# Kernel optimization log

Hardware: AMD Instinct MI355X
Metric: run time of the kernel (lower is better)

## Reference

```python
import jax, jax.numpy as jnp
import numpy as np

VOCAB, EMBED, HIDDEN, NCLS = 32000, 512, 1024, 1000
BATCH, SEQ = 128, 512


def setup_inputs() -> dict:
    key = jax.random.key(0)
    ks = jax.random.split(key, 8)
    s_in = 1.0 / np.sqrt(EMBED + HIDDEN)
    s_h = 1.0 / np.sqrt(HIDDEN)
    return {
        "x": jax.random.randint(ks[0], (BATCH, SEQ), 0, VOCAB, dtype=jnp.int32),
        "emb": jax.random.normal(ks[1], (VOCAB, EMBED), dtype=jnp.float32),
        "Wz": jax.random.uniform(ks[2], (EMBED + HIDDEN, HIDDEN), jnp.float32, -s_in, s_in),
        "bz": jax.random.uniform(ks[3], (HIDDEN,), jnp.float32, -s_in, s_in),
        "Wh": jax.random.uniform(ks[4], (EMBED + HIDDEN, HIDDEN), jnp.float32, -s_in, s_in),
        "bh": jax.random.uniform(ks[5], (HIDDEN,), jnp.float32, -s_in, s_in),
        "Wfc": jax.random.uniform(ks[6], (HIDDEN, NCLS), jnp.float32, -s_h, s_h),
        "bfc": jax.random.uniform(ks[7], (NCLS,), jnp.float32, -s_h, s_h),
    }


def reference(x, emb, Wz, bz, Wh, bh, Wfc, bfc):
    # embedding lookup: [B, S, E]
    e = emb[x]
    B = x.shape[0]
    h0 = jnp.zeros((B, Wz.shape[1]), dtype=emb.dtype)

    def step(h, x_t):
        c = jnp.concatenate([x_t, h], axis=1)          # [B, E+H]
        z = jax.nn.sigmoid(c @ Wz + bz)                # forget/update gate
        h_tilde = jnp.tanh(c @ Wh + bh)                # candidate state
        h_new = (1.0 - z) * h + z * h_tilde
        return h_new, None

    h_final, _ = jax.lax.scan(step, h0, jnp.swapaxes(e, 0, 1))  # scan over S
    return h_final @ Wfc + bfc                          # logits [B, NCLS]
```

## Files before the change

kernel.cpp:

```cpp
#include <hip/hip_runtime.h>

#define BATCH 128
#define SEQ   512
#define EMB   512
#define HID   1024
#define NCLS  1000
#define NBLK  128
#define TPB   512

using short8 = __attribute__((ext_vector_type(8))) short;
using f32x4  = __attribute__((ext_vector_type(4))) float;
typedef unsigned long long u64;

__device__ __forceinline__ short f2bf(float f) {
    unsigned u = __float_as_uint(f);
    unsigned r = (u + 0x7fffu + ((u >> 16) & 1u)) >> 16;
    return (short)r;
}
__device__ __forceinline__ float bf2f(short s) {
    unsigned u = ((unsigned)(unsigned short)s) << 16;
    return __uint_as_float(u);
}
__device__ __forceinline__ short8 pack8(float4 a, float4 b) {
    short8 s;
    s[0] = f2bf(a.x); s[1] = f2bf(a.y); s[2] = f2bf(a.z); s[3] = f2bf(a.w);
    s[4] = f2bf(b.x); s[5] = f2bf(b.y); s[6] = f2bf(b.z); s[7] = f2bf(b.w);
    return s;
}
__device__ __forceinline__ short8 mk8(u64 lo, u64 hi) {
    union { u64 d[2]; short8 s; } u;
    u.d[0] = lo; u.d[1] = hi;
    return u.s;
}

#define OFF_CH0 0u
#define OFF_CL0 262144u
#define OFF_BAR 524288u
#define OFF_CH1 526336u
#define OFF_CL1 788480u
#define OFF_H   1050624u
#define ZERO_I4 32896u

__global__ void mgu_init(int4* __restrict__ ws4) {
    unsigned i = blockIdx.x * blockDim.x + threadIdx.x;
    if (i < ZERO_I4) ws4[i] = make_int4(0, 0, 0, 0);
}

__global__ __launch_bounds__(TPB, 1) void mgu_scan(
    const int* __restrict__ x, const float* __restrict__ emb,
    const float* __restrict__ Wz, const float* __restrict__ bz,
    const float* __restrict__ Wh, const float* __restrict__ bh,
    short* __restrict__ ch0, short* __restrict__ cl0,
    short* __restrict__ ch1, short* __restrict__ cl1,
    unsigned* __restrict__ bars, float* __restrict__ h)
{
    __shared__ f32x4 Rbuf[8][8][64];
    __shared__ short TrH[8][16][8];
    __shared__ short TrL[8][16][8];

    const int tid  = threadIdx.x;
    const int w    = tid >> 6;
    const int lane = tid & 63;
    const int q    = lane >> 4;
    const int n    = lane & 15;
    const int blk  = blockIdx.x;
    const int r0   = (blk >> 4) << 4;
    const int jb   = (blk & 15) << 6;
    const int j0   = jb + (w << 3);
    const int frg  = (blk >> 4) * 16384;
    const int ksw  = ((blk & 15) << 1) + (w >> 2);
    const int qw   = w & 3;
    unsigned* bar  = bars + ((blk >> 4) << 6);

    const float* Wg = (n < 8) ? Wz : Wh;
    short8 Bf[48];
#pragma unroll
    for (int c = 0; c < 8; ++c) {
#pragma unroll
        for (int m = 0; m < 6; ++m) {
            const float* wp = Wg + jb + (c << 3) + (n & 7);
            short8 f;
#pragma unroll
            for (int i = 0; i < 8; ++i)
                f[i] = f2bf(wp[(long)((w + 8 * m) * 32 + q * 8 + i) * HID]);
            Bf[c * 6 + m] = f;
        }
    }
    const float bzv = bz[j0 + (n & 7)];
    const float bhv = bh[j0 + (n & 7)];

    float hreg[4] = {0.f, 0.f, 0.f, 0.f};

    const int xrow = (r0 + n) * SEQ;
    const int eoff = (w << 5) + (q << 3);

    short8 fe0, fe1;
    {
        int tok = x[xrow];
        const float* ep = emb + (long)tok * EMB + eoff;
        float4 a0 = *(const float4*)(ep);
        float4 a1 = *(const float4*)(ep + 4);
        float4 b0 = *(const float4*)(ep + 256);
        float4 b1 = *(const float4*)(ep + 260);
        fe0 = pack8(a0, a1);
        fe1 = pack8(b0, b1);
    }

    for (int t = 0; t < SEQ; ++t) {
        const short* chR = (t & 1) ? ch1 : ch0;
        const short* clR = (t & 1) ? cl1 : cl0;
        short*       chW = (t & 1) ? ch0 : ch1;
        short*       clW = (t & 1) ? cl0 : cl1;

        int tok_nxt = x[xrow + ((t < SEQ - 1) ? t + 1 : t)];

        u64 hh[8], ll[8];
#pragma unroll
        for (int mm = 0; mm < 4; ++mm) {
            const u64* hp = (const u64*)(chR + frg + (w + 8 * mm) * 512 + (lane << 2));
            hh[2 * mm]     = __hip_atomic_load(hp,      __ATOMIC_RELAXED, __HIP_MEMORY_SCOPE_AGENT);
            hh[2 * mm + 1] = __hip_atomic_load(hp + 64, __ATOMIC_RELAXED, __HIP_MEMORY_SCOPE_AGENT);
        }
#pragma unroll
        for (int mm = 0; mm < 4; ++mm) {
            const u64* lp = (const u64*)(clR + frg + (w + 8 * mm) * 512 + (lane << 2));
            ll[2 * mm]     = __hip_atomic_load(lp,      __ATOMIC_RELAXED, __HIP_MEMORY_SCOPE_AGENT);
            ll[2 * mm + 1] = __hip_atomic_load(lp + 64, __ATOMIC_RELAXED, __HIP_MEMORY_SCOPE_AGENT);
        }

        f32x4 acc[8];
#pragma unroll
        for (int c = 0; c < 8; ++c) acc[c] = (f32x4){0.f, 0.f, 0.f, 0.f};

#pragma unroll
        for (int c = 0; c < 8; ++c)
            acc[c] = __builtin_amdgcn_mfma_f32_16x16x32_bf16(fe0, Bf[c * 6 + 0], acc[c], 0, 0, 0);
#pragma unroll
        for (int c = 0; c < 8; ++c)
            acc[c] = __builtin_amdgcn_mfma_f32_16x16x32_bf16(fe1, Bf[c * 6 + 1], acc[c], 0, 0, 0);

#pragma unroll
        for (int mm = 0; mm < 4; ++mm) {
            short8 fh = mk8(hh[2 * mm], hh[2 * mm + 1]);
#pragma unroll
            for (int c = 0; c < 8; ++c)
                acc[c] = __builtin_amdgcn_mfma_f32_16x16x32_bf16(fh, Bf[c * 6 + 2 + mm], acc[c], 0, 0, 0);
        }
#pragma unroll
        for (int mm = 0; mm < 4; ++mm) {
            short8 fl = mk8(ll[2 * mm], ll[2 * mm + 1]);
#pragma unroll
            for (int c = 0; c < 8; ++c)
                acc[c] = __builtin_amdgcn_mfma_f32_16x16x32_bf16(fl, Bf[c * 6 + 2 + mm], acc[c], 0, 0, 0);
        }

#pragma unroll
        for (int c = 0; c < 8; ++c) Rbuf[w][c][lane] = acc[c];
        __syncthreads();
        f32x4 r = Rbuf[0][w][lane];
#pragma unroll
        for (int w2 = 1; w2 < 8; ++w2) r += Rbuf[w2][w][lane];

        float oarr[4];
        oarr[0] = __shfl_xor(r[0], 8, 64);
        oarr[1] = __shfl_xor(r[1], 8, 64);
        oarr[2] = __shfl_xor(r[2], 8, 64);
        oarr[3] = __shfl_xor(r[3], 8, 64);

        if (n < 8) {
            const int j = j0 + n;
#pragma unroll
            for (int r2 = 0; r2 < 4; ++r2) {
                float z  = 1.f / (1.f + __expf(-(r[r2] + bzv)));
                float ht = tanhf(oarr[r2] + bhv);
                float ho = hreg[r2];
                float hn = ho + z * (ht - ho);
                hreg[r2] = hn;
                if (t < SEQ - 1) {
                    short hi = f2bf(hn);
                    TrH[w][q * 4 + r2][n] = hi;
                    TrL[w][q * 4 + r2][n] = f2bf(hn - bf2f(hi));
                } else {
                    h[(r0 + q * 4 + r2) * HID + j] = hn;
                }
            }
        }

        if (t < SEQ - 1) {
            __syncthreads();
            if (lane < 32) {
                const int p = lane >> 4, rr = lane & 15;
                u64 vh = *(const u64*)&TrH[w][rr][p << 2];
                u64 vl = *(const u64*)&TrL[w][rr][p << 2];
                const int off = frg + ksw * 512 + (p << 8) + (((qw << 4) + rr) << 2);
                __hip_atomic_store((u64*)(chW + off), vh, __ATOMIC_RELAXED, __HIP_MEMORY_SCOPE_AGENT);
                __hip_atomic_store((u64*)(clW + off), vl, __ATOMIC_RELAXED, __HIP_MEMORY_SCOPE_AGENT);
            }
            __syncthreads();
            if (tid == 0)
                __hip_atomic_fetch_add(bar, 1u, __ATOMIC_RELAXED, __HIP_MEMORY_SCOPE_AGENT);
            {
                const float* ep = emb + (long)tok_nxt * EMB + eoff;
                float4 a0 = *(const float4*)(ep);
                float4 a1 = *(const float4*)(ep + 4);
                float4 b0 = *(const float4*)(ep + 256);
                float4 b1 = *(const float4*)(ep + 260);
                fe0 = pack8(a0, a1);
                fe1 = pack8(b0, b1);
            }
            if (tid == 0) {
                unsigned tgt = (unsigned)(t + 1) * 16u;
                while (__hip_atomic_load(bar, __ATOMIC_RELAXED, __HIP_MEMORY_SCOPE_AGENT) < tgt)
                    __builtin_amdgcn_s_sleep(1);
            }
            __syncthreads();
        }
    }
}

__global__ __launch_bounds__(256) void mgu_fc(const float* __restrict__ h,
                                              const float* __restrict__ Wfc,
                                              const float* __restrict__ bfc,
                                              float* __restrict__ out) {
    __shared__ float hs[BATCH][65];
    const int tid = threadIdx.x;
    const int n0  = blockIdx.x * 8;
    const int b   = tid & 127;
    const int nn  = tid >> 7;
    const int nc  = n0 + nn * 4;
    float acc0 = 0.f, acc1 = 0.f, acc2 = 0.f, acc3 = 0.f;

    for (int k0 = 0; k0 < HID; k0 += 64) {
        __syncthreads();
#pragma unroll
        for (int jj = 0; jj < 8; ++jj) {
            int idx = tid + jj * 256;
            int bb  = idx >> 4;
            int kk  = (idx & 15) << 2;
            const float4 v = *(const float4*)(h + bb * HID + k0 + kk);
            hs[bb][kk] = v.x; hs[bb][kk + 1] = v.y; hs[bb][kk + 2] = v.z; hs[bb][kk + 3] = v.w;
        }
        __syncthreads();
#pragma unroll 8
        for (int k = 0; k < 64; ++k) {
            float hv = hs[b][k];
            const float4 wv = *(const float4*)(Wfc + (long)(k0 + k) * NCLS + nc);
            acc0 += hv * wv.x; acc1 += hv * wv.y; acc2 += hv * wv.z; acc3 += hv * wv.w;
        }
    }
    float* op = out + b * NCLS + nc;
    op[0] = acc0 + bfc[nc + 0];
    op[1] = acc1 + bfc[nc + 1];
    op[2] = acc2 + bfc[nc + 2];
    op[3] = acc3 + bfc[nc + 3];
}

extern "C" void kernel_launch(void* const* d_in, const int* in_sizes, int n_in,
                              void* d_out, int out_size, void* d_ws, size_t ws_size,
                              hipStream_t stream) {
    const int*   x   = (const int*)  d_in[0];
    const float* emb = (const float*)d_in[1];
    const float* Wz  = (const float*)d_in[2];
    const float* bz  = (const float*)d_in[3];
    const float* Wh  = (const float*)d_in[4];
    const float* bh  = (const float*)d_in[5];
    const float* Wfc = (const float*)d_in[6];
    const float* bfc = (const float*)d_in[7];
    float* out = (float*)d_out;

    char* ws = (char*)d_ws;
    short*    ch0  = (short*)   (ws + OFF_CH0);
    short*    cl0  = (short*)   (ws + OFF_CL0);
    unsigned* bars = (unsigned*)(ws + OFF_BAR);
    short*    ch1  = (short*)   (ws + OFF_CH1);
    short*    cl1  = (short*)   (ws + OFF_CL1);
    float*    h    = (float*)   (ws + OFF_H);

    mgu_init<<<129, 256, 0, stream>>>((int4*)ws);

    mgu_scan<<<NBLK, TPB, 0, stream>>>(x, emb, Wz, bz, Wh, bh,
                                       ch0, cl0, ch1, cl1, bars, h);

    mgu_fc<<<125, 256, 0, stream>>>(h, Wfc, bfc, out);
}
```

Baseline: 3.521 ms.

## Replace group-wide atomic barrier with per-wave producer flags and fine-grained waits

Swaps the per-row-group counter barrier (a fetch_add followed by one thread spinning, plus several block-wide syncthreads) for per-wave flags. Each wave publishes its slice of h with a flag store, and each consumer wave polls only the flags of the slices it reads. The input-embedding MFMAs are moved ahead of the wait so they overlap the dependency, and Rbuf is double-buffered so some syncthreads can be dropped. The aim is to cut barrier latency on the serial 512-step recurrence. The risk is memory-ordering subtlety, since the relaxed flag store is ordered only by s_waitcnt, and heavier polling traffic from 64 lanes per wave.

```diff
diff --git a/kernel.cpp b/kernel.cpp
--- a/kernel.cpp
+++ b/kernel.cpp
@@ -35,11 +35,11 @@
 
 #define OFF_CH0 0u
 #define OFF_CL0 262144u
-#define OFF_BAR 524288u
-#define OFF_CH1 526336u
-#define OFF_CL1 788480u
-#define OFF_H   1050624u
-#define ZERO_I4 32896u
+#define OFF_FLG 524288u
+#define OFF_CH1 528384u
+#define OFF_CL1 790528u
+#define OFF_H   1052672u
+#define ZERO_I4 33024u
 
 __global__ void mgu_init(int4* __restrict__ ws4) {
     unsigned i = blockIdx.x * blockDim.x + threadIdx.x;
@@ -52,9 +52,9 @@
     const float* __restrict__ Wh, const float* __restrict__ bh,
     short* __restrict__ ch0, short* __restrict__ cl0,
     short* __restrict__ ch1, short* __restrict__ cl1,
-    unsigned* __restrict__ bars, float* __restrict__ h)
+    unsigned* __restrict__ flags, float* __restrict__ h)
 {
-    __shared__ f32x4 Rbuf[8][8][64];
+    __shared__ f32x4 Rbuf[2][8][8][64];
     __shared__ short TrH[8][16][8];
     __shared__ short TrL[8][16][8];
 
@@ -70,7 +70,9 @@
     const int frg  = (blk >> 4) * 16384;
     const int ksw  = ((blk & 15) << 1) + (w >> 2);
     const int qw   = w & 3;
-    unsigned* bar  = bars + ((blk >> 4) << 6);
+    unsigned* flbase = flags + ((blk >> 4) << 7);
+    unsigned* flw  = flbase + (ksw << 2) + qw;
+    const unsigned* flp = flbase + (w << 2) + (((lane & 15) >> 2) << 5) + (lane & 3);
 
     const float* Wg = (n < 8) ? Wz : Wh;
     short8 Bf[48];
@@ -114,6 +116,25 @@
 
         int tok_nxt = x[xrow + ((t < SEQ - 1) ? t + 1 : t)];
 
+        f32x4 acc[8];
+#pragma unroll
+        for (int c = 0; c < 8; ++c) acc[c] = (f32x4){0.f, 0.f, 0.f, 0.f};
+
+#pragma unroll
+        for (int c = 0; c < 8; ++c)
+            acc[c] = __builtin_amdgcn_mfma_f32_16x16x32_bf16(fe0, Bf[c * 6 + 0], acc[c], 0, 0, 0);
+#pragma unroll
+        for (int c = 0; c < 8; ++c)
+            acc[c] = __builtin_amdgcn_mfma_f32_16x16x32_bf16(fe1, Bf[c * 6 + 1], acc[c], 0, 0, 0);
+
+        {
+            const unsigned want = (unsigned)t;
+            unsigned fv;
+            do {
+                fv = __hip_atomic_load(flp, __ATOMIC_RELAXED, __HIP_MEMORY_SCOPE_AGENT);
+            } while (!__all((int)(fv >= want)));
+        }
+
         u64 hh[8], ll[8];
 #pragma unroll
         for (int mm = 0; mm < 4; ++mm) {
@@ -128,17 +149,6 @@
             ll[2 * mm + 1] = __hip_atomic_load(lp + 64, __ATOMIC_RELAXED, __HIP_MEMORY_SCOPE_AGENT);
         }
 
-        f32x4 acc[8];
-#pragma unroll
-        for (int c = 0; c < 8; ++c) acc[c] = (f32x4){0.f, 0.f, 0.f, 0.f};
-
-#pragma unroll
-        for (int c = 0; c < 8; ++c)
-            acc[c] = __builtin_amdgcn_mfma_f32_16x16x32_bf16(fe0, Bf[c * 6 + 0], acc[c], 0, 0, 0);
-#pragma unroll
-        for (int c = 0; c < 8; ++c)
-            acc[c] = __builtin_amdgcn_mfma_f32_16x16x32_bf16(fe1, Bf[c * 6 + 1], acc[c], 0, 0, 0);
-
 #pragma unroll
         for (int mm = 0; mm < 4; ++mm) {
             short8 fh = mk8(hh[2 * mm], hh[2 * mm + 1]);
@@ -155,11 +165,11 @@
         }
 
 #pragma unroll
-        for (int c = 0; c < 8; ++c) Rbuf[w][c][lane] = acc[c];
+        for (int c = 0; c < 8; ++c) Rbuf[t & 1][w][c][lane] = acc[c];
         __syncthreads();
-        f32x4 r = Rbuf[0][w][lane];
-#pragma unroll
-        for (int w2 = 1; w2 < 8; ++w2) r += Rbuf[w2][w][lane];
+        f32x4 r = Rbuf[t & 1][0][w][lane];
+#pragma unroll
+        for (int w2 = 1; w2 < 8; ++w2) r += Rbuf[t & 1][w2][w][lane];
 
         float oarr[4];
         oarr[0] = __shfl_xor(r[0], 8, 64);
@@ -187,7 +197,6 @@
         }
 
         if (t < SEQ - 1) {
-            __syncthreads();
             if (lane < 32) {
                 const int p = lane >> 4, rr = lane & 15;
                 u64 vh = *(const u64*)&TrH[w][rr][p << 2];
@@ -196,24 +205,17 @@
                 __hip_atomic_store((u64*)(chW + off), vh, __ATOMIC_RELAXED, __HIP_MEMORY_SCOPE_AGENT);
                 __hip_atomic_store((u64*)(clW + off), vl, __ATOMIC_RELAXED, __HIP_MEMORY_SCOPE_AGENT);
             }
-            __syncthreads();
-            if (tid == 0)
-                __hip_atomic_fetch_add(bar, 1u, __ATOMIC_RELAXED, __HIP_MEMORY_SCOPE_AGENT);
-            {
-                const float* ep = emb + (long)tok_nxt * EMB + eoff;
-                float4 a0 = *(const float4*)(ep);
-                float4 a1 = *(const float4*)(ep + 4);
-                float4 b0 = *(const float4*)(ep + 256);
-                float4 b1 = *(const float4*)(ep + 260);
-                fe0 = pack8(a0, a1);
-                fe1 = pack8(b0, b1);
-            }
-            if (tid == 0) {
-                unsigned tgt = (unsigned)(t + 1) * 16u;
-                while (__hip_atomic_load(bar, __ATOMIC_RELAXED, __HIP_MEMORY_SCOPE_AGENT) < tgt)
-                    __builtin_amdgcn_s_sleep(1);
-            }
-            __syncthreads();
+            asm volatile("s_waitcnt vmcnt(0)" ::: "memory");
+            if (lane == 0)
+                __hip_atomic_store(flw, (unsigned)(t + 1),
+                                   __ATOMIC_RELAXED, __HIP_MEMORY_SCOPE_AGENT);
+            const float* ep = emb + (long)tok_nxt * EMB + eoff;
+            float4 a0 = *(const float4*)(ep);
+            float4 a1 = *(const float4*)(ep + 4);
+            float4 b0 = *(const float4*)(ep + 256);
+            float4 b1 = *(const float4*)(ep + 260);
+            fe0 = pack8(a0, a1);
+            fe1 = pack8(b0, b1);
         }
     }
 }
@@ -269,17 +271,17 @@
     float* out = (float*)d_out;
 
     char* ws = (char*)d_ws;
-    short*    ch0  = (short*)   (ws + OFF_CH0);
-    short*    cl0  = (short*)   (ws + OFF_CL0);
-    unsigned* bars = (unsigned*)(ws + OFF_BAR);
-    short*    ch1  = (short*)   (ws + OFF_CH1);
-    short*    cl1  = (short*)   (ws + OFF_CL1);
-    float*    h    = (float*)   (ws + OFF_H);
+    short*    ch0   = (short*)   (ws + OFF_CH0);
+    short*    cl0   = (short*)   (ws + OFF_CL0);
+    unsigned* flags = (unsigned*)(ws + OFF_FLG);
+    short*    ch1   = (short*)   (ws + OFF_CH1);
+    short*    cl1   = (short*)   (ws + OFF_CL1);
+    float*    h     = (float*)   (ws + OFF_H);
 
     mgu_init<<<129, 256, 0, stream>>>((int4*)ws);
 
     mgu_scan<<<NBLK, TPB, 0, stream>>>(x, emb, Wz, bz, Wh, bh,
-                                       ch0, cl0, ch1, cl1, bars, h);
+                                       ch0, cl0, ch1, cl1, flags, h);
 
     mgu_fc<<<125, 256, 0, stream>>>(h, Wfc, bfc, out);
 }
```

After: 3.758 ms. +6.7%, slower.
